# Kernel tuning notes

Hardware: AMD Instinct MI355X
Metric: run time of the kernel (lower is better)

Reference implementation:

```python
import jax, jax.numpy as jnp
import numpy as np

# static sizes (see shape_source)
IN_SIZE = 50000
M = 3            # n_modalities
N0 = 40960       # layer-0 sampled source nodes
N1 = 16384       # layer-0 dst == layer-1 src
B = 4096         # batch (final dst nodes)
HEADS = 4
DIM = 64
HD = HEADS * DIM # 256, integration_size
DEG0, DEG1 = 16, 16
E0, E1 = N1 * DEG0, B * DEG1
NEG_SLOPE = 0.2  # GATConv default negative_slope


def gat_conv(x_src, e_src, e_dst, n_dst, W, att, bias):
    """PyG GATConv with bipartite input (x, None): attention uses only alpha_l.
    x_src: [Ns, HD]; W: [HD, HD]; att: [1, H, C]; returns [n_dst, HD]."""
    x_l = (x_src @ W.T).reshape(-1, HEADS, DIM)            # [Ns, H, C]
    alpha_l = (x_l * att).sum(-1)                          # [Ns, H]
    logits = jax.nn.leaky_relu(alpha_l[e_src], NEG_SLOPE)  # [E, H]
    m = jax.ops.segment_max(logits, e_dst, num_segments=n_dst)
    m = jnp.where(jnp.isfinite(m), m, 0.0)                 # guard empty segments
    e = jnp.exp(logits - m[e_dst])
    denom = jax.ops.segment_sum(e, e_dst, num_segments=n_dst)
    a = e / (denom[e_dst] + 1e-16)                         # edge softmax per dst
    msg = x_l[e_src] * a[:, :, None]                       # [E, H, C]
    out = jax.ops.segment_sum(msg, e_dst, num_segments=n_dst)
    return out.reshape(n_dst, HD) + bias


def interp(scales_param, mask, key):
    """Interp module, evaluate=False, idxs = range(M)."""
    scales = jax.nn.softmax(scales_param, axis=-1)         # [1, M]
    rm = jax.random.randint(key, mask.shape, 0, 2).astype(jnp.float32)
    rm = rm + (1.0 / (1.0 + rm.sum(-1)) ** 20)[:, None]
    rm = rm + (1.0 / (mask.sum(-1) ** 20))[:, None]
    rm = jax.lax.stop_gradient(jnp.floor(rm))              # .int().float()
    rm = rm / (rm + 1e-10)
    m = mask * rm
    m = jax.nn.softmax(m + (1.0 - m) * (-1e10), axis=-1)   # [B, M]
    return scales, m


def setup_inputs() -> dict:
    key = jax.random.key(0)
    ks = jax.random.split(key, 12)
    s = 0.05
    return {
        "masks": jnp.ones((B, M), jnp.float32),
        "n_ids": jax.random.randint(ks[0], (M, N0), 0, IN_SIZE, dtype=jnp.int32),
        "e0_src": jax.random.randint(ks[1], (M, E0), 0, N0, dtype=jnp.int32),
        "e0_dst": jnp.repeat(jnp.arange(N1, dtype=jnp.int32), DEG0),
        "e1_src": jax.random.randint(ks[2], (M, E1), 0, N1, dtype=jnp.int32),
        "e1_dst": jnp.repeat(jnp.arange(B, dtype=jnp.int32), DEG1),
        "pre_W": jax.random.normal(ks[3], (M, HD, IN_SIZE), jnp.float32) * s,
        "pre_b": jax.random.normal(ks[4], (M, HD), jnp.float32) * s,
        "gat_W": jax.random.normal(ks[5], (M, HD, HD), jnp.float32) * s,
        "gat_att": jax.random.normal(ks[6], (M, 1, HEADS, DIM), jnp.float32) * s,
        "gat_b": jax.random.normal(ks[7], (M, HD), jnp.float32) * s,
        "scales_param": jnp.full((1, M), 1.0 / M, jnp.float32),
        "emb_W": jax.random.normal(ks[8], (128, HD), jnp.float32) * s,
        "emb_b": jax.random.normal(ks[9], (128,), jnp.float32) * s,
    }


def reference(masks, n_ids, e0_src, e0_dst, e1_src, e1_dst,
              pre_W, pre_b, gat_W, gat_att, gat_b,
              scales_param, emb_W, emb_b):
    scales, interp_masks = interp(scales_param, masks, jax.random.key(42))
    x_mod = jnp.zeros((B, HD), dtype=masks.dtype)
    for i in range(M):  # small fixed modality loop (structurally distinct params)
        # one-hot(n_id) @ W.T + b  ==  gather of columns of W (same math)
        x = jnp.take(pre_W[i], n_ids[i], axis=1).T + pre_b[i]        # [N0, HD]
        g0 = gat_conv(x, e0_src[i], e0_dst, N1, gat_W[i], gat_att[i], gat_b[i])
        g1 = gat_conv(g0, e1_src[i], e1_dst, B, gat_W[i], gat_att[i], gat_b[i])
        # x_store_layer = [g0[:B] (sliced), g0[:B] (x_pre), g1]; x = sum + g1
        xm = 2.0 * g0[:B] + 2.0 * g1                                  # [B, HD]
        xm = scales[:, i] * interp_masks[:, i].reshape(-1, 1) * xm
        x_mod = x_mod + xm
    emb = x_mod @ emb_W.T + emb_b                                     # [B, 128]
    dot = emb @ emb.T                                                 # [B, B]
    return dot, emb, scales
```

## Files before the change

### kernel.cpp

```cpp
#include <hip/hip_runtime.h>
#include <hip/hip_bf16.h>
#include <cstdint>

#define IN_SZ 50000
#define PADC  50048
#define NM 3
#define N0 40960
#define N1 16384
#define NB 4096
#define HD 256
#define DEG 16
#define E0 (N1*DEG)
#define E1 (NB*DEG)

using short8v = __attribute__((ext_vector_type(8))) short;
using floatx4 = __attribute__((ext_vector_type(4))) float;
typedef unsigned short ushort_t;

__device__ __forceinline__ ushort_t f2bf(float f){
  uint32_t u = __float_as_uint(f);
  uint32_t r = u + 0x7FFFu + ((u>>16)&1u);
  return (ushort_t)(r>>16);
}
__device__ __forceinline__ float bf2f(ushort_t h){
  return __uint_as_float(((uint32_t)h)<<16);
}
__device__ __forceinline__ void gload_lds16(const void* g, void* l){
  __builtin_amdgcn_global_load_lds(
      (const __attribute__((address_space(1))) void*)g,
      (__attribute__((address_space(3))) void*)l, 16, 0, 0);
}

__device__ __forceinline__ uint32_t rotl32(uint32_t x, uint32_t d){ return (x<<d)|(x>>(32u-d)); }

__device__ void tf2x32(uint32_t k0, uint32_t k1, uint32_t c0, uint32_t c1,
                       uint32_t& y0, uint32_t& y1)
{
  uint32_t ks2 = k0 ^ k1 ^ 0x1BD11BDAu;
  uint32_t x0 = c0 + k0, x1 = c1 + k1;
#define R4(a,b,c,d) \
  x0+=x1; x1=rotl32(x1,a); x1^=x0; \
  x0+=x1; x1=rotl32(x1,b); x1^=x0; \
  x0+=x1; x1=rotl32(x1,c); x1^=x0; \
  x0+=x1; x1=rotl32(x1,d); x1^=x0;
  R4(13,15,26,6)  x0+=k1;  x1+=ks2+1u;
  R4(17,29,16,24) x0+=ks2; x1+=k0+2u;
  R4(13,15,26,6)  x0+=k0;  x1+=k1+3u;
  R4(17,29,16,24) x0+=k1;  x1+=ks2+4u;
  R4(13,15,26,6)  x0+=ks2; x1+=k0+5u;
#undef R4
  y0=x0; y1=x1;
}

__global__ __launch_bounds__(256) void prep_k(
    const float* __restrict__ masks, const float* __restrict__ sp,
    float* __restrict__ coef, float* __restrict__ scales_out,
    const float* __restrict__ emb_W, float* __restrict__ wT,
    const float* __restrict__ gat_W, ushort_t* __restrict__ gWhi, ushort_t* __restrict__ gWlo,
    const float* __restrict__ pre_b, const float* __restrict__ gat_att,
    const float* __restrict__ gat_b, float* __restrict__ bsum, float* __restrict__ batt,
    float* __restrict__ watt)
{
  int blk = blockIdx.x;
  int t = threadIdx.x;
  if (blk < 16){
    int b = blk*256 + t;
    float s0=sp[0], s1=sp[1], s2=sp[2];
    float mx = fmaxf(s0,fmaxf(s1,s2));
    float e0=expf(s0-mx), e1=expf(s1-mx), e2=expf(s2-mx);
    float inv = 1.f/(e0+e1+e2);
    float sc[3] = {e0*inv, e1*inv, e2*inv};
    if (b == 0){ scales_out[0]=sc[0]; scales_out[1]=sc[1]; scales_out[2]=sc[2]; }
    uint32_t bits[3];
    uint32_t K0,K1, t0,t1;
    tf2x32(0u,42u,0u,1u,K0,K1);
    for (int i=0;i<3;i++){
      uint32_t idx = (uint32_t)(b*3+i);
      tf2x32(K0,K1,0u,idx,t0,t1);
      bits[i] = (t0 ^ t1) & 1u;
    }
    float mk[3] = {masks[b*3+0], masks[b*3+1], masks[b*3+2]};
    float msum = mk[0]+mk[1]+mk[2];
    float rs = (float)(bits[0]+bits[1]+bits[2]);
    float add = powf(1.f/(1.f+rs), 20.f) + powf(1.f/msum, 20.f);
    float lg[3]; float lmax = -1e30f;
    for (int i=0;i<3;i++){
      float rm = floorf((float)bits[i] + add);
      rm = rm/(rm+1e-10f);
      float mm = mk[i]*rm;
      lg[i] = mm + (1.f-mm)*(-1e10f);
      lmax = fmaxf(lmax, lg[i]);
    }
    float es[3], ssum=0.f;
    for (int i=0;i<3;i++){ es[i]=expf(lg[i]-lmax); ssum+=es[i]; }
    for (int i=0;i<3;i++) coef[b*3+i] = sc[i]*es[i]/ssum;
  } else if (blk < 144){
    int g = (blk-16)*256 + t;
    int j = g >> 8, k = g & 255;
    wT[k*128 + j] = emb_W[g];
  } else if (blk < 912){
    int g = (blk-144)*256 + t;
    float v = gat_W[g];
    ushort_t h = f2bf(v);
    gWhi[g] = h;
    gWlo[g] = f2bf(v - bf2f(h));
  } else if (blk < 915){
    int i = blk - 912, o = t;
    const float* W = gat_W + (size_t)i*HD*HD + (size_t)o*HD;
    const float* b = pre_b + i*HD;
    float s = 0.f;
    for (int k=0;k<HD;k++) s = fmaf(b[k], W[k], s);
    bsum[i*HD + o] = s + gat_b[i*HD + o];
    __shared__ float red[256];
    red[o] = s * gat_att[i*HD + o];
    __syncthreads();
    if (o < 4){
      float p = 0.f;
      for (int j=0;j<64;j++) p += red[o*64 + j];
      batt[i*4 + o] = p;
    }
  } else {
    int idx = blk - 915;
    int i = idx >> 2, h = idx & 3;
    int k = t;
    float s = 0.f;
    for (int o=0;o<64;o++){
      int oo = h*64 + o;
      s = fmaf(gat_W[(size_t)i*HD*HD + (size_t)oo*HD + k], gat_att[i*HD + oo], s);
    }
    watt[(size_t)i*1024 + k*4 + h] = s;
  }
}

__global__ __launch_bounds__(256) void transp4_k(const float* __restrict__ Wb,
                                                 ushort_t* __restrict__ WT_b)
{
  int i = blockIdx.z;
  const float* W = Wb + (size_t)i*HD*IN_SZ;
  ushort_t* WT = WT_b + (size_t)i*(size_t)PADC*HD;
  __shared__ float tile[32][33];
  int c0 = blockIdx.x*32, k0 = blockIdx.y*32;
  int t = threadIdx.x;
  int lk = t>>3, lq = t&7;
  int cbase = c0 + lq*4;
  float4 f;
  if (cbase + 3 < IN_SZ){
    f = *reinterpret_cast<const float4*>(&W[(size_t)(k0+lk)*IN_SZ + cbase]);
  } else {
    float tmp[4] = {0.f,0.f,0.f,0.f};
#pragma unroll
    for (int e=0;e<4;e++) if (cbase+e < IN_SZ) tmp[e] = W[(size_t)(k0+lk)*IN_SZ + cbase+e];
    f = make_float4(tmp[0],tmp[1],tmp[2],tmp[3]);
  }
  tile[lk][lq*4+0]=f.x; tile[lk][lq*4+1]=f.y; tile[lk][lq*4+2]=f.z; tile[lk][lq*4+3]=f.w;
  __syncthreads();
  int sc = t>>3, skq = t&7;
  uint32_t lo = (uint32_t)f2bf(tile[skq*4+0][sc]) | ((uint32_t)f2bf(tile[skq*4+1][sc])<<16);
  uint32_t hi = (uint32_t)f2bf(tile[skq*4+2][sc]) | ((uint32_t)f2bf(tile[skq*4+3][sc])<<16);
  uint2 pack = make_uint2(lo, hi);
  *reinterpret_cast<uint2*>(&WT[(size_t)(c0+sc)*HD + k0 + skq*4]) = pack;
}

__global__ __launch_bounds__(64) void msg0agg(
    const ushort_t* __restrict__ WT_b, const int* __restrict__ n_ids,
    const int* __restrict__ esrc_b, const float* __restrict__ watt_b,
    const float* __restrict__ batt, ushort_t* __restrict__ agg_b)
{
  int i = blockIdx.y, d = blockIdx.x, lane = threadIdx.x;
  const ushort_t* WT = WT_b + (size_t)i*(size_t)PADC*HD;
  __shared__ uint32_t rows[16*129];
  __shared__ float wl[1024];
  __shared__ float aw_s[64];
  __shared__ int src_s[16];
  if (lane < 16) src_s[lane] = n_ids[(size_t)i*N0 + esrc_b[(size_t)i*E0 + d*16 + lane]];
  const float* wg = watt_b + (size_t)i*1024;
#pragma unroll
  for (int j=0;j<16;j++) wl[j*64 + lane] = wg[j*64 + lane];
  __syncthreads();
#pragma unroll
  for (int e=0;e<16;e++){
    const uint32_t* rp = reinterpret_cast<const uint32_t*>(WT + (size_t)src_s[e]*HD);
    rows[e*129 + lane]      = rp[lane];
    rows[e*129 + 64 + lane] = rp[64 + lane];
  }
  __syncthreads();
  int e = lane>>2, h = lane&3;
  float dot = 0.f;
  for (int j=0;j<128;j++){
    uint32_t u = rows[e*129 + j];
    dot = fmaf(bf2f((ushort_t)(u & 0xffffu)), wl[(2*j)*4 + h], dot);
    dot = fmaf(bf2f((ushort_t)(u >> 16)),     wl[(2*j+1)*4 + h], dot);
  }
  dot += batt[i*4 + h];
  float l = dot > 0.f ? dot : 0.2f*dot;
  float m = l;
#pragma unroll
  for (int off=4; off<64; off<<=1) m = fmaxf(m, __shfl_xor(m, off, 64));
  float ex = expf(l - m);
  float s = ex;
#pragma unroll
  for (int off=4; off<64; off<<=1) s += __shfl_xor(s, off, 64);
  aw_s[lane] = ex / (s + 1e-16f);
  __syncthreads();
  int hh = lane >> 4;
  float a0=0.f,a1=0.f,a2=0.f,a3=0.f;
#pragma unroll
  for (int e2=0;e2<16;e2++){
    float w = aw_s[e2*4 + hh];
    uint32_t u0 = rows[e2*129 + 2*lane];
    uint32_t u1 = rows[e2*129 + 2*lane + 1];
    a0 = fmaf(w, bf2f((ushort_t)(u0 & 0xffffu)), a0);
    a1 = fmaf(w, bf2f((ushort_t)(u0 >> 16)), a1);
    a2 = fmaf(w, bf2f((ushort_t)(u1 & 0xffffu)), a2);
    a3 = fmaf(w, bf2f((ushort_t)(u1 >> 16)), a3);
  }
  uint32_t p0 = (uint32_t)f2bf(a0) | ((uint32_t)f2bf(a1)<<16);
  uint32_t p1 = (uint32_t)f2bf(a2) | ((uint32_t)f2bf(a3)<<16);
  uint32_t* op = reinterpret_cast<uint32_t*>(agg_b + ((size_t)i*N1 + d)*HD);
  op[2*lane] = p0; op[2*lane+1] = p1;
}

template<bool BIASMODE>
__global__ __launch_bounds__(256) void gemm2(
    const ushort_t* __restrict__ A_b, size_t a_stride,
    const ushort_t* __restrict__ Whi_b, const ushort_t* __restrict__ Wlo_b,
    ushort_t* __restrict__ C_b, size_t c_stride,
    const float* __restrict__ att_b, float* __restrict__ alpha_b, size_t al_stride,
    const float* __restrict__ bias_b)
{
  int i = blockIdx.z;
  int bn0 = blockIdx.x * 128;
  int brow = blockIdx.y * 128;
  const ushort_t* A = A_b + (size_t)i*a_stride;
  const ushort_t* Whi = Whi_b + (size_t)i*HD*HD;
  const ushort_t* Wlo = Wlo_b + (size_t)i*HD*HD;
  ushort_t* C = C_b + (size_t)i*c_stride;

  __shared__ __align__(16) ushort_t smem[2][24*512];
  int t = threadIdx.x, wave = t>>6, lane = t&63;
  int l15 = lane&15, kq = lane>>4;

  int row0 = brow + wave*16 + l15;
  int row1 = brow + (wave+4)*16 + l15;

  const ushort_t* gsrc[6];
  gsrc[0] = A + (size_t)row0*HD + kq*8;
  gsrc[1] = A + (size_t)row1*HD + kq*8;
#pragma unroll
  for (int j=2;j<6;j++){
    int idx = wave + 4*(j-2);
    int ct = idx>>1, h = idx&1;
    const ushort_t* W = h ? Wlo : Whi;
    gsrc[j] = W + (size_t)(bn0 + ct*16 + l15)*HD + kq*8;
  }

  floatx4 acc[4][4];
#pragma unroll
  for (int r=0;r<4;r++)
#pragma unroll
    for (int c=0;c<4;c++) acc[r][c] = (floatx4){0.f,0.f,0.f,0.f};

  int wm = wave>>1, wn = wave&1;

#pragma unroll
  for (int j=0;j<6;j++)
    gload_lds16(gsrc[j], &smem[0][(wave + 4*j)*512] + lane*8);
  __syncthreads();

  for (int cc=0; cc<8; cc++){
    int buf = cc & 1;
    if (cc < 7){
      int k0 = (cc+1)*32;
#pragma unroll
      for (int j=0;j<6;j++)
        gload_lds16(gsrc[j] + k0, &smem[buf^1][(wave + 4*j)*512] + lane*8);
    }
    short8v a[4];
#pragma unroll
    for (int r=0;r<4;r++)
      a[r] = *reinterpret_cast<const short8v*>(&smem[buf][(wm*4+r)*512 + lane*8]);
#pragma unroll
    for (int c=0;c<4;c++){
      int ct = wn*4+c;
      short8v bh = *reinterpret_cast<const short8v*>(&smem[buf][(8+ct*2)*512 + lane*8]);
      short8v bl = *reinterpret_cast<const short8v*>(&smem[buf][(9+ct*2)*512 + lane*8]);
#pragma unroll
      for (int r=0;r<4;r++){
        acc[r][c] = __builtin_amdgcn_mfma_f32_16x16x32_bf16(a[r], bh, acc[r][c], 0,0,0);
        acc[r][c] = __builtin_amdgcn_mfma_f32_16x16x32_bf16(a[r], bl, acc[r][c], 0,0,0);
      }
    }
    __syncthreads();
  }

  float attv[4];
#pragma unroll
  for (int c=0;c<4;c++){
    int col = bn0 + (wn*4+c)*16 + l15;
    if constexpr (BIASMODE) attv[c] = bias_b[i*HD + col];
    else                    attv[c] = att_b[(size_t)i*HD + col];
  }
  int head = (bn0>>6) + wn;
#pragma unroll
  for (int r=0;r<4;r++){
    int rowb = brow + wm*64 + r*16 + kq*4;
#pragma unroll
    for (int j=0;j<4;j++){
      size_t rw = (size_t)(rowb + j)*HD;
#pragma unroll
      for (int c=0;c<4;c++){
        float v = acc[r][c][j];
        if constexpr (BIASMODE) v += attv[c];
        C[rw + bn0 + (wn*4+c)*16 + l15] = f2bf(v);
      }
    }
    if constexpr (!BIASMODE){
#pragma unroll
      for (int j=0;j<4;j++){
        float p = acc[r][0][j]*attv[0] + acc[r][1][j]*attv[1]
                + acc[r][2][j]*attv[2] + acc[r][3][j]*attv[3];
        p += __shfl_xor(p, 1, 64);
        p += __shfl_xor(p, 2, 64);
        p += __shfl_xor(p, 4, 64);
        p += __shfl_xor(p, 8, 64);
        if (l15 == 0){
          float lg = p > 0.f ? p : 0.2f*p;
          alpha_b[(size_t)i*al_stride + (size_t)(rowb + j)*4 + head] = lg;
        }
      }
    }
  }
}

__global__ __launch_bounds__(128) void gat_msg1(
    const ushort_t* __restrict__ xl1hi, const float* __restrict__ alpha1,
    const int* __restrict__ e1src, const float* __restrict__ gat_b,
    const uint32_t* __restrict__ g0_u, const float* __restrict__ coef,
    float* __restrict__ xmod)
{
  int d = blockIdx.x, t = threadIdx.x;
  __shared__ int src[16];
  __shared__ float aw[16][4];
  float o0 = 0.f, o1 = 0.f;
  for (int i=0;i<NM;i++){
    if (t < 16) src[t] = e1src[(size_t)i*E1 + d*16 + t];
    __syncthreads();
    if (t < 64){
      int e = t&15, h = t>>4;
      float l = alpha1[((size_t)i*N1 + src[e])*4 + h];
      float m = l;
#pragma unroll
      for (int off=1; off<16; off<<=1) m = fmaxf(m, __shfl_xor(m, off, 64));
      float ex = expf(l - m);
      float s = ex;
#pragma unroll
      for (int off=1; off<16; off<<=1) s += __shfl_xor(s, off, 64);
      aw[e][h] = ex / (s + 1e-16f);
    }
    __syncthreads();
    const ushort_t* xl = xl1hi + (size_t)i*N1*HD;
    int h = t >> 5;
    float a0=0.f, a1=0.f;
#pragma unroll
    for (int e=0;e<16;e++){
      uint32_t u = *reinterpret_cast<const uint32_t*>(xl + (size_t)src[e]*HD + 2*t);
      float w = aw[e][h];
      a0 = fmaf(w, bf2f((ushort_t)(u & 0xffffu)), a0);
      a1 = fmaf(w, bf2f((ushort_t)(u >> 16)), a1);
    }
    uint32_t gh = g0_u[((size_t)i*N1 + d)*128 + t];
    float g00 = bf2f((ushort_t)(gh & 0xffffu));
    float g01 = bf2f((ushort_t)(gh >> 16));
    const float* bias = gat_b + i*HD;
    float cv = coef[d*3 + i];
    o0 += cv*(2.f*g00 + 2.f*(a0 + bias[2*t]));
    o1 += cv*(2.f*g01 + 2.f*(a1 + bias[2*t+1]));
    __syncthreads();
  }
  *reinterpret_cast<float2*>(&xmod[(size_t)d*HD + 2*t]) = make_float2(o0, o1);
}

__global__ __launch_bounds__(256) void emb_gemm(
  const float* __restrict__ xmod, const float* __restrict__ wT,
  const float* __restrict__ eb, float* __restrict__ emb,
  ushort_t* __restrict__ ehi, ushort_t* __restrict__ elo)
{
  __shared__ float xs[32][260];
  int t = threadIdx.x;
  int brow = blockIdx.x * 32;
#pragma unroll
  for (int j=0;j<8;j++){
    int linear = j*256+t;
    int row = linear >> 6;
    int kq = linear & 63;
    float4 f = *reinterpret_cast<const float4*>(&xmod[(size_t)(brow+row)*256 + kq*4]);
    xs[row][kq*4+0]=f.x; xs[row][kq*4+1]=f.y; xs[row][kq*4+2]=f.z; xs[row][kq*4+3]=f.w;
  }
  __syncthreads();
  int tj = t & 127, th = t >> 7;
  float acc[16];
#pragma unroll
  for(int r=0;r<16;r++) acc[r]=0.f;
  for (int k=0;k<256;k++){
    float w = wT[k*128 + tj];
#pragma unroll
    for (int r=0;r<16;r++) acc[r] = fmaf(xs[th*16+r][k], w, acc[r]);
  }
  float bias = eb[tj];
#pragma unroll
  for (int r=0;r<16;r++){
    size_t idx = (size_t)(brow+th*16+r)*128 + tj;
    float v = acc[r] + bias;
    emb[idx] = v;
    ushort_t hb = f2bf(v);
    ehi[idx] = hb;
    elo[idx] = f2bf(v - bf2f(hb));
  }
}

__global__ __launch_bounds__(256) void dot_mfma(
    const ushort_t* __restrict__ Ehi, const ushort_t* __restrict__ Elo,
    float* __restrict__ dot)
{
  __shared__ __align__(16) ushort_t lb[2][16384];
  int t = threadIdx.x, wave = t>>6, lane = t&63;
  int arow0 = blockIdx.y*128, brow0 = blockIdx.x*128;
  {
    const ushort_t* srcp = (t<128) ? Ehi : Elo;
    ushort_t* dstb = lb[(t<128)?0:1];
    int o = t & 127;
    const ushort_t* rp = srcp + (size_t)(brow0+o)*128;
#pragma unroll
    for (int g=0; g<16; g++){
      short8v v = *reinterpret_cast<const short8v*>(rp + g*8);
      int c = g>>2, grp = g&3;
      int lidx = c*4096 + (o>>4)*512 + ((grp<<4)|(o&15))*8;
      *reinterpret_cast<short8v*>(&dstb[lidx]) = v;
    }
  }
  __syncthreads();

  floatx4 acc[2][8];
#pragma unroll
  for (int rt=0;rt<2;rt++)
#pragma unroll
    for (int ot=0;ot<8;ot++) acc[rt][ot] = (floatx4){0.f,0.f,0.f,0.f};

  int ar0 = arow0 + wave*32 + (lane&15);
  int ar1 = ar0 + 16;
  int koff = (lane>>4)*8;
#pragma unroll
  for (int c=0;c<4;c++){
    short8v ah0 = *reinterpret_cast<const short8v*>(Ehi + (size_t)ar0*128 + c*32 + koff);
    short8v ah1 = *reinterpret_cast<const short8v*>(Ehi + (size_t)ar1*128 + c*32 + koff);
    short8v al0 = *reinterpret_cast<const short8v*>(Elo + (size_t)ar0*128 + c*32 + koff);
    short8v al1 = *reinterpret_cast<const short8v*>(Elo + (size_t)ar1*128 + c*32 + koff);
#pragma unroll
    for (int ot=0;ot<8;ot++){
      short8v bh = *reinterpret_cast<const short8v*>(&lb[0][c*4096 + ot*512 + lane*8]);
      short8v bl = *reinterpret_cast<const short8v*>(&lb[1][c*4096 + ot*512 + lane*8]);
      acc[0][ot] = __builtin_amdgcn_mfma_f32_16x16x32_bf16(ah0, bh, acc[0][ot], 0,0,0);
      acc[0][ot] = __builtin_amdgcn_mfma_f32_16x16x32_bf16(ah0, bl, acc[0][ot], 0,0,0);
      acc[0][ot] = __builtin_amdgcn_mfma_f32_16x16x32_bf16(al0, bh, acc[0][ot], 0,0,0);
      acc[1][ot] = __builtin_amdgcn_mfma_f32_16x16x32_bf16(ah1, bh, acc[1][ot], 0,0,0);
      acc[1][ot] = __builtin_amdgcn_mfma_f32_16x16x32_bf16(ah1, bl, acc[1][ot], 0,0,0);
      acc[1][ot] = __builtin_amdgcn_mfma_f32_16x16x32_bf16(al1, bh, acc[1][ot], 0,0,0);
    }
  }
#pragma unroll
  for (int rt=0;rt<2;rt++){
    int rb = arow0 + wave*32 + rt*16 + (lane>>4)*4;
#pragma unroll
    for (int r=0;r<4;r++)
#pragma unroll
      for (int ot=0;ot<8;ot++)
        dot[(size_t)(rb+r)*4096 + brow0 + ot*16 + (lane&15)] = acc[rt][ot][r];
  }
}

extern "C" void kernel_launch(void* const* d_in, const int* in_sizes, int n_in,
                              void* d_out, int out_size, void* d_ws, size_t ws_size,
                              hipStream_t stream) {
  (void)in_sizes; (void)n_in; (void)out_size; (void)ws_size;
  const float* masks   = (const float*)d_in[0];
  const int*   n_ids   = (const int*)d_in[1];
  const int*   e0_src  = (const int*)d_in[2];
  const int*   e1_src  = (const int*)d_in[4];
  const float* pre_W   = (const float*)d_in[6];
  const float* pre_b   = (const float*)d_in[7];
  const float* gat_W   = (const float*)d_in[8];
  const float* gat_att = (const float*)d_in[9];
  const float* gat_b   = (const float*)d_in[10];
  const float* sp      = (const float*)d_in[11];
  const float* emb_W   = (const float*)d_in[12];
  const float* emb_b   = (const float*)d_in[13];

  float* out = (float*)d_out;
  float* dot = out;
  float* emb = out + (size_t)NB*NB;
  float* scales_out = emb + (size_t)NB*128;

  char* p = (char*)d_ws;
  auto alloc = [&](size_t bytes)->char*{ char* r = p; p += (bytes + 255) & ~(size_t)255; return r; };
  ushort_t* WT    = (ushort_t*)alloc((size_t)NM*PADC*HD*2);
  ushort_t* agg   = (ushort_t*)alloc((size_t)NM*N1*HD*2);
  uint32_t* g0u   = (uint32_t*)alloc((size_t)NM*N1*HD*2);
  ushort_t* xl1hi = (ushort_t*)alloc((size_t)NM*N1*HD*2);
  float*    alph1 = (float*)alloc((size_t)NM*N1*4*4);
  float*    xmod  = (float*)alloc((size_t)NB*HD*4);
  float*    coef  = (float*)alloc((size_t)NB*3*4);
  float*    wT    = (float*)alloc((size_t)HD*128*4);
  ushort_t* gWhi  = (ushort_t*)alloc((size_t)NM*HD*HD*2);
  ushort_t* gWlo  = (ushort_t*)alloc((size_t)NM*HD*HD*2);
  float*    bsum  = (float*)alloc((size_t)NM*HD*4);
  float*    batt  = (float*)alloc((size_t)NM*4*4);
  float*    watt  = (float*)alloc((size_t)NM*1024*4);
  ushort_t* ehi   = (ushort_t*)alloc((size_t)NB*128*2);
  ushort_t* elo   = (ushort_t*)alloc((size_t)NB*128*2);

  prep_k<<<927, 256, 0, stream>>>(masks, sp, coef, scales_out, emb_W, wT,
                                  gat_W, gWhi, gWlo, pre_b, gat_att, gat_b,
                                  bsum, batt, watt);
  transp4_k<<<dim3(PADC/32, 8, NM), 256, 0, stream>>>(pre_W, WT);
  msg0agg<<<dim3(N1, NM), 64, 0, stream>>>(WT, n_ids, e0_src, watt, batt, agg);
  gemm2<true><<<dim3(2, N1/128, NM), 256, 0, stream>>>(
      agg, (size_t)N1*HD, gWhi, gWlo,
      (ushort_t*)g0u, (size_t)N1*HD, nullptr, nullptr, 0, bsum);
  gemm2<false><<<dim3(2, N1/128, NM), 256, 0, stream>>>(
      (const ushort_t*)g0u, (size_t)N1*HD, gWhi, gWlo,
      xl1hi, (size_t)N1*HD, gat_att, alph1, (size_t)N1*4, nullptr);
  gat_msg1<<<NB, 128, 0, stream>>>(xl1hi, alph1, e1_src, gat_b, g0u, coef, xmod);
  emb_gemm<<<NB/32, 256, 0, stream>>>(xmod, wT, emb_b, emb, ehi, elo);
  dot_mfma<<<dim3(32,32), 256, 0, stream>>>(ehi, elo, dot);
}
```

Baseline: 288.5 us.

## Precompute per-column attention logits and simplify layer-0 message aggregation

Splits the layer-0 gather kernel into a per-vocabulary-column attention logit kernel and a lighter aggregation kernel. Logits were previously recomputed for each of 16 edges per destination. Now they are computed once per column and gathered, which cuts redundant dot products. The aggregation kernel reads rows straight from global memory without shared-memory staging. The trade-off is an extra launch and computing logits for columns that may be unused.

```diff
diff --git a/kernel.cpp b/kernel.cpp
--- a/kernel.cpp
+++ b/kernel.cpp
@@ -161,63 +161,90 @@
   *reinterpret_cast<uint2*>(&WT[(size_t)(c0+sc)*HD + k0 + skq*4]) = pack;
 }
 
-__global__ __launch_bounds__(64) void msg0agg(
-    const ushort_t* __restrict__ WT_b, const int* __restrict__ n_ids,
-    const int* __restrict__ esrc_b, const float* __restrict__ watt_b,
-    const float* __restrict__ batt, ushort_t* __restrict__ agg_b)
-{
-  int i = blockIdx.y, d = blockIdx.x, lane = threadIdx.x;
+__global__ __launch_bounds__(256) void alphaG_k(
+    const ushort_t* __restrict__ WT_b, const float* __restrict__ watt_b,
+    const float* __restrict__ batt, float* __restrict__ alphaG_b)
+{
+  int i = blockIdx.y;
+  int row0 = blockIdx.x * 64;
   const ushort_t* WT = WT_b + (size_t)i*(size_t)PADC*HD;
-  __shared__ uint32_t rows[16*129];
+  float* alphaG = alphaG_b + (size_t)i*(size_t)PADC*4;
   __shared__ float wl[1024];
-  __shared__ float aw_s[64];
-  __shared__ int src_s[16];
-  if (lane < 16) src_s[lane] = n_ids[(size_t)i*N0 + esrc_b[(size_t)i*E0 + d*16 + lane]];
-  const float* wg = watt_b + (size_t)i*1024;
-#pragma unroll
-  for (int j=0;j<16;j++) wl[j*64 + lane] = wg[j*64 + lane];
-  __syncthreads();
+  int t = threadIdx.x;
+  {
+    const float* wg = watt_b + (size_t)i*1024;
+#pragma unroll
+    for (int j=0;j<4;j++) wl[j*256 + t] = wg[j*256 + t];
+  }
+  __syncthreads();
+  int row = row0 + (t>>2), part = t&3;
+  const uint2* rp = reinterpret_cast<const uint2*>(WT + (size_t)row*HD + part*64);
+  float p0=0.f,p1=0.f,p2=0.f,p3=0.f;
+#pragma unroll
+  for (int j=0;j<16;j++){
+    uint2 u = rp[j];
+    int k = part*64 + 4*j;
+    float v0 = bf2f((ushort_t)(u.x & 0xffffu));
+    float v1 = bf2f((ushort_t)(u.x >> 16));
+    float v2 = bf2f((ushort_t)(u.y & 0xffffu));
+    float v3 = bf2f((ushort_t)(u.y >> 16));
+    p0 = fmaf(v0, wl[(k+0)*4+0], p0); p1 = fmaf(v0, wl[(k+0)*4+1], p1);
+    p2 = fmaf(v0, wl[(k+0)*4+2], p2); p3 = fmaf(v0, wl[(k+0)*4+3], p3);
+    p0 = fmaf(v1, wl[(k+1)*4+0], p0); p1 = fmaf(v1, wl[(k+1)*4+1], p1);
+    p2 = fmaf(v1, wl[(k+1)*4+2], p2); p3 = fmaf(v1, wl[(k+1)*4+3], p3);
+    p0 = fmaf(v2, wl[(k+2)*4+0], p0); p1 = fmaf(v2, wl[(k+2)*4+1], p1);
+    p2 = fmaf(v2, wl[(k+2)*4+2], p2); p3 = fmaf(v2, wl[(k+2)*4+3], p3);
+    p0 = fmaf(v3, wl[(k+3)*4+0], p0); p1 = fmaf(v3, wl[(k+3)*4+1], p1);
+    p2 = fmaf(v3, wl[(k+3)*4+2], p2); p3 = fmaf(v3, wl[(k+3)*4+3], p3);
+  }
+#pragma unroll
+  for (int off=1; off<4; off<<=1){
+    p0 += __shfl_xor(p0, off, 64);
+    p1 += __shfl_xor(p1, off, 64);
+    p2 += __shfl_xor(p2, off, 64);
+    p3 += __shfl_xor(p3, off, 64);
+  }
+  float s = (part==0) ? p0 : (part==1) ? p1 : (part==2) ? p2 : p3;
+  s += batt[i*4 + part];
+  alphaG[(size_t)row*4 + part] = s > 0.f ? s : 0.2f*s;
+}
+
+__global__ __launch_bounds__(128) void gat_msg0w(
+    const ushort_t* __restrict__ WT_b, const float* __restrict__ alphaG_b,
+    const int* __restrict__ n_ids, const int* __restrict__ esrc_b,
+    ushort_t* __restrict__ agg_b)
+{
+  int i = blockIdx.y, d = blockIdx.x, t = threadIdx.x;
+  const ushort_t* WT = WT_b + (size_t)i*(size_t)PADC*HD;
+  const float* alphaG = alphaG_b + (size_t)i*(size_t)PADC*4;
+  __shared__ int src[16];
+  __shared__ float aw[16][4];
+  if (t < 16) src[t] = n_ids[(size_t)i*N0 + esrc_b[(size_t)i*E0 + d*16 + t]];
+  __syncthreads();
+  if (t < 64){
+    int e = t&15, h = t>>4;
+    float l = alphaG[(size_t)src[e]*4 + h];
+    float m = l;
+#pragma unroll
+    for (int off=1; off<16; off<<=1) m = fmaxf(m, __shfl_xor(m, off, 64));
+    float ex = expf(l - m);
+    float s = ex;
+#pragma unroll
+    for (int off=1; off<16; off<<=1) s += __shfl_xor(s, off, 64);
+    aw[e][h] = ex / (s + 1e-16f);
+  }
+  __syncthreads();
+  int h = t >> 5;
+  float a0=0.f, a1=0.f;
 #pragma unroll
   for (int e=0;e<16;e++){
-    const uint32_t* rp = reinterpret_cast<const uint32_t*>(WT + (size_t)src_s[e]*HD);
-    rows[e*129 + lane]      = rp[lane];
-    rows[e*129 + 64 + lane] = rp[64 + lane];
-  }
-  __syncthreads();
-  int e = lane>>2, h = lane&3;
-  float dot = 0.f;
-  for (int j=0;j<128;j++){
-    uint32_t u = rows[e*129 + j];
-    dot = fmaf(bf2f((ushort_t)(u & 0xffffu)), wl[(2*j)*4 + h], dot);
-    dot = fmaf(bf2f((ushort_t)(u >> 16)),     wl[(2*j+1)*4 + h], dot);
-  }
-  dot += batt[i*4 + h];
-  float l = dot > 0.f ? dot : 0.2f*dot;
-  float m = l;
-#pragma unroll
-  for (int off=4; off<64; off<<=1) m = fmaxf(m, __shfl_xor(m, off, 64));
-  float ex = expf(l - m);
-  float s = ex;
-#pragma unroll
-  for (int off=4; off<64; off<<=1) s += __shfl_xor(s, off, 64);
-  aw_s[lane] = ex / (s + 1e-16f);
-  __syncthreads();
-  int hh = lane >> 4;
-  float a0=0.f,a1=0.f,a2=0.f,a3=0.f;
-#pragma unroll
-  for (int e2=0;e2<16;e2++){
-    float w = aw_s[e2*4 + hh];
-    uint32_t u0 = rows[e2*129 + 2*lane];
-    uint32_t u1 = rows[e2*129 + 2*lane + 1];
-    a0 = fmaf(w, bf2f((ushort_t)(u0 & 0xffffu)), a0);
-    a1 = fmaf(w, bf2f((ushort_t)(u0 >> 16)), a1);
-    a2 = fmaf(w, bf2f((ushort_t)(u1 & 0xffffu)), a2);
-    a3 = fmaf(w, bf2f((ushort_t)(u1 >> 16)), a3);
-  }
-  uint32_t p0 = (uint32_t)f2bf(a0) | ((uint32_t)f2bf(a1)<<16);
-  uint32_t p1 = (uint32_t)f2bf(a2) | ((uint32_t)f2bf(a3)<<16);
-  uint32_t* op = reinterpret_cast<uint32_t*>(agg_b + ((size_t)i*N1 + d)*HD);
-  op[2*lane] = p0; op[2*lane+1] = p1;
+    uint32_t u = *reinterpret_cast<const uint32_t*>(WT + (size_t)src[e]*HD + 2*t);
+    float w = aw[e][h];
+    a0 = fmaf(w, bf2f((ushort_t)(u & 0xffffu)), a0);
+    a1 = fmaf(w, bf2f((ushort_t)(u >> 16)), a1);
+  }
+  uint32_t pk = (uint32_t)f2bf(a0) | ((uint32_t)f2bf(a1)<<16);
+  reinterpret_cast<uint32_t*>(agg_b + ((size_t)i*N1 + d)*HD)[t] = pk;
 }
 
 template<bool BIASMODE>
@@ -503,6 +530,7 @@
   char* p = (char*)d_ws;
   auto alloc = [&](size_t bytes)->char*{ char* r = p; p += (bytes + 255) & ~(size_t)255; return r; };
   ushort_t* WT    = (ushort_t*)alloc((size_t)NM*PADC*HD*2);
+  float*    alphG = (float*)alloc((size_t)NM*PADC*4*4);
   ushort_t* agg   = (ushort_t*)alloc((size_t)NM*N1*HD*2);
   uint32_t* g0u   = (uint32_t*)alloc((size_t)NM*N1*HD*2);
   ushort_t* xl1hi = (ushort_t*)alloc((size_t)NM*N1*HD*2);
@@ -522,7 +550,8 @@
                                   gat_W, gWhi, gWlo, pre_b, gat_att, gat_b,
                                   bsum, batt, watt);
   transp4_k<<<dim3(PADC/32, 8, NM), 256, 0, stream>>>(pre_W, WT);
-  msg0agg<<<dim3(N1, NM), 64, 0, stream>>>(WT, n_ids, e0_src, watt, batt, agg);
+  alphaG_k<<<dim3(PADC/64, NM), 256, 0, stream>>>(WT, watt, batt, alphG);
+  gat_msg0w<<<dim3(N1, NM), 128, 0, stream>>>(WT, alphG, n_ids, e0_src, agg);
   gemm2<true><<<dim3(2, N1/128, NM), 256, 0, stream>>>(
       agg, (size_t)N1*HD, gWhi, gWlo,
       (ushort_t*)g0u, (size_t)N1*HD, nullptr, nullptr, 0, bsum);
```

Result: faster. 262.0 us (-9.2%).
